# Performance work log

Measured on AMD Instinct MI355X. Metric: run time of the kernel, lower is better.

## Reference

```python
import jax, jax.numpy as jnp
import numpy as np

NEG_INF = -1e12  # matches masked_fill value -1000000000000.0
LEAKY_SLOPE = 0.2


def setup_inputs() -> dict:
    key = jax.random.key(0)
    k1, k2, k3, k4, k5 = jax.random.split(key, 5)
    B, C, H, N, F_IN, F_OUT = 4, 4, 4, 1024, 64, 64
    h = jax.random.normal(k1, (B, C, N, F_IN), dtype=jnp.float32)
    adj = jax.random.randint(k2, (B, N, N), 0, 2).astype(jnp.float32)
    w = jax.random.normal(k3, (C, H, F_IN, F_OUT), dtype=jnp.float32) * 0.1
    a_src = jax.random.normal(k4, (C, H, F_OUT, 1), dtype=jnp.float32) * 0.1
    a_dst = jax.random.normal(k5, (C, H, F_OUT, 1), dtype=jnp.float32) * 0.1
    return {"h": h, "adj": adj, "w": w, "a_src": a_src, "a_dst": a_dst}


def reference(h, adj, w, a_src, a_dst):
    # h: [B,C,N,f_in], w: [C,H,f_in,f_out] -> h_prime: [B,C,H,N,f_out]
    h_prime = jnp.einsum('bcnf,chfo->bchno', h, w)
    t = jnp.tanh(h_prime)
    # additive attention scores: [B,C,H,N]
    attn_src = jnp.einsum('bchno,cho->bchn', t, a_src[..., 0])
    attn_dst = jnp.einsum('bchno,cho->bchn', t, a_dst[..., 0])
    # attn[b,c,h,i,j] = src[i] + dst[j]  -> [B,C,H,N,N]
    attn = attn_src[..., :, None] + attn_dst[..., None, :]
    attn = jnp.where(attn >= 0, attn, LEAKY_SLOPE * attn)  # leaky_relu(0.2)
    N = h.shape[2]
    adj_sl = adj + jnp.eye(N, dtype=adj.dtype)  # add self-loops
    mask = (adj_sl == 0)[:, None, None, :, :]   # [B,1,1,N,N]
    attn = jnp.where(mask, NEG_INF, attn)
    attn = jax.nn.softmax(attn, axis=-1)
    # dropout is identity (attn_dropout=0.0 / eval mode)
    out = jnp.einsum('bchnm,bchmo->bchno', attn, h_prime)
    return out
```

## Files before the change

### kernel.cpp

```cpp
#include <hip/hip_runtime.h>
#include <hip/hip_bf16.h>
#include <math.h>

#define NB 4
#define NC 4
#define NH 4
#define NN 1024
#define NF 64
#define NCOMBO 64
#define LEAK 0.2f

typedef __attribute__((ext_vector_type(8)))  short  short8;
typedef __attribute__((ext_vector_type(16))) float  float16;

static __device__ __forceinline__ unsigned pk_bf16(float a, float b) {
    union { __hip_bfloat162 h; unsigned u; } cv;
    cv.h = __float22bfloat162_rn(make_float2(a, b));
    return cv.u;
}

static __device__ __forceinline__ float fast_tanh(float x) {
    const float e = __expf(2.f * x);
    return 1.f - 2.f * __builtin_amdgcn_rcpf(1.f + e);
}

static __device__ __forceinline__ float mask_by_bit(float p, unsigned bb, int k) {
#if defined(__has_builtin) && __has_builtin(__builtin_amdgcn_sbfe)
    const int m = __builtin_amdgcn_sbfe((int)bb, k, 1);
#else
    const int m = -(int)((bb >> k) & 1u);
#endif
    union { float f; int i; } u;
    u.f = p; u.i &= m;
    return u.f;
}

static __device__ __forceinline__ void split8(const float4 a, const float4 b,
                                              short8* hi, short8* lo) {
    union { short8 v; unsigned u[4]; } H, L;
    const float x[8] = {a.x,a.y,a.z,a.w,b.x,b.y,b.z,b.w};
    float lov[8];
    #pragma unroll
    for (int p = 0; p < 4; ++p) {
        const unsigned pk = pk_bf16(x[2*p], x[2*p+1]);
        H.u[p] = pk;
        union { unsigned u; float f; } f0, f1;
        f0.u = pk << 16; f1.u = pk & 0xffff0000u;
        lov[2*p]   = x[2*p]   - f0.f;
        lov[2*p+1] = x[2*p+1] - f1.f;
    }
    #pragma unroll
    for (int p = 0; p < 4; ++p) L.u[p] = pk_bf16(lov[2*p], lov[2*p+1]);
    *hi = H.v; *lo = L.v;
}

__global__ __launch_bounds__(256) void gA_produce(
    const float* __restrict__ h, const float* __restrict__ adj,
    const float* __restrict__ w, const float* __restrict__ a_src,
    const float* __restrict__ a_dst,
    unsigned short* __restrict__ hpt, float* __restrict__ asrc,
    float* __restrict__ edPt, float* __restrict__ edNt,
    unsigned long long* __restrict__ bits)
{
    __shared__ __align__(16) char smem[17920];
    float* w_s    = (float*)smem;
    unsigned short* whi = (unsigned short*)smem;
    unsigned short* wlo = (unsigned short*)(smem + 8192);
    float* as_lds = (float*)(smem + 16384);
    float* ad_lds = (float*)(smem + 16640);
    float* scS    = (float*)(smem + 16896);
    float* scD    = (float*)(smem + 17408);

    const int idx  = blockIdx.x;
    const int t    = threadIdx.x;
    const int g    = (idx & 7)*8 + ((idx >> 3) & 7);
    const int tile = idx >> 6;
    const int b = g >> 4, c = (g >> 2) & 3, hh = g & 3;
    const int lane = t & 63, l31 = lane & 31, half = lane >> 5;
    const int wv = t >> 6, rg = wv >> 1, oh = wv & 1;

    const float4* wsrc = (const float4*)(w + ((size_t)(c*NH + hh))*NF*NF);
    #pragma unroll
    for (int i = 0; i < 4; ++i)
        ((float4*)w_s)[t + i*256] = wsrc[t + i*256];
    if (t < NF) {
        as_lds[t] = a_src[(c*NH + hh)*NF + t];
        ad_lds[t] = a_dst[(c*NH + hh)*NF + t];
    }
    __syncthreads();

    float wv0[8], wv1[8];
    {
        const int n = t & 31;
        #pragma unroll
        for (int j = 0; j < 8; ++j) {
            const int blk0 = t >> 5, blk1 = (t >> 5) + 8;
            const int k0 = (blk0 >> 2)*16 + (blk0 & 1)*8 + j;
            const int o0 = ((blk0 >> 1) & 1)*32 + n;
            const int k1 = (blk1 >> 2)*16 + (blk1 & 1)*8 + j;
            const int o1 = ((blk1 >> 1) & 1)*32 + n;
            wv0[j] = w_s[k0*64 + o0];
            wv1[j] = w_s[k1*64 + o1];
        }
    }
    short8 ahi[4], alo[4];
    {
        const float* hrow = h +
            (((size_t)(b*NC + c))*NN + tile*64 + rg*32 + l31)*NF;
        #pragma unroll
        for (int s = 0; s < 4; ++s) {
            const float4 v0 = *(const float4*)&hrow[s*16 + half*8];
            const float4 v1 = *(const float4*)&hrow[s*16 + half*8 + 4];
            split8(v0, v1, &ahi[s], &alo[s]);
        }
    }
    __syncthreads();

    {
        union { short8 v; unsigned u[4]; } H; short8 L;
        float4 a0 = make_float4(wv0[0],wv0[1],wv0[2],wv0[3]);
        float4 a1 = make_float4(wv0[4],wv0[5],wv0[6],wv0[7]);
        split8(a0, a1, &H.v, &L);
        *(short8*)&whi[((t >> 5)*32 + (t & 31))*8] = H.v;
        *(short8*)&wlo[((t >> 5)*32 + (t & 31))*8] = L;
        a0 = make_float4(wv1[0],wv1[1],wv1[2],wv1[3]);
        a1 = make_float4(wv1[4],wv1[5],wv1[6],wv1[7]);
        split8(a0, a1, &H.v, &L);
        *(short8*)&whi[(((t >> 5) + 8)*32 + (t & 31))*8] = H.v;
        *(short8*)&wlo[(((t >> 5) + 8)*32 + (t & 31))*8] = L;
    }
    __syncthreads();

    float16 acc;
    #pragma unroll
    for (int i = 0; i < 16; ++i) acc[i] = 0.f;
    #pragma unroll
    for (int s = 0; s < 4; ++s) {
        const short8 bhi = *(const short8*)&whi[(((s*2 + oh)*2 + half)*32 + l31)*8];
        const short8 blo = *(const short8*)&wlo[(((s*2 + oh)*2 + half)*32 + l31)*8];
        acc = __builtin_amdgcn_mfma_f32_32x32x16_bf16(ahi[s], bhi, acc, 0, 0, 0);
        acc = __builtin_amdgcn_mfma_f32_32x32x16_bf16(alo[s], bhi, acc, 0, 0, 0);
        acc = __builtin_amdgcn_mfma_f32_32x32x16_bf16(ahi[s], blo, acc, 0, 0, 0);
    }

    {
        const int col = oh*32 + l31;
        const float av = as_lds[col], dv = ad_lds[col];
        float sS[16], sD[16];
        #pragma unroll
        for (int reg = 0; reg < 16; ++reg) {
            const float tt = fast_tanh(acc[reg]);
            sS[reg] = tt * av;
            sD[reg] = tt * dv;
        }
        #pragma unroll
        for (int off = 1; off <= 16; off <<= 1) {
            #pragma unroll
            for (int reg = 0; reg < 16; ++reg) {
                sS[reg] += __shfl_xor(sS[reg], off);
                sD[reg] += __shfl_xor(sD[reg], off);
            }
        }
        if (l31 == 0) {
            #pragma unroll
            for (int reg = 0; reg < 16; ++reg) {
                const int row = rg*32 + (reg & 3) + 8*(reg >> 2) + 4*half;
                scS[row*2 + oh] = sS[reg];
                scD[row*2 + oh] = sD[reg];
            }
        }
    }

    {
        unsigned short* dst = hpt + ((size_t)(g*16 + tile))*4096;
        #pragma unroll
        for (int q = 0; q < 4; ++q) {
            const int ks = rg*2 + (q >> 1), hf = q & 1;
            const int elem = (((ks*2 + oh)*2 + hf)*32 + l31)*8 + 4*half;
            uint2 pk;
            pk.x = pk_bf16(acc[q*4 + 0], acc[q*4 + 1]);
            pk.y = pk_bf16(acc[q*4 + 2], acc[q*4 + 3]);
            *(uint2*)&dst[elem] = pk;
        }
    }
    __syncthreads();
    if (t < 64) {
        const float s = scS[t*2] + scS[t*2 + 1];
        const float d = scD[t*2] + scD[t*2 + 1];
        asrc[(size_t)g*NN + tile*64 + t] = s;
        edPt[(size_t)g*NN + tile*64 + t] = __expf(d);
        edNt[(size_t)g*NN + tile*64 + t] = __expf(LEAK*d);
    }

    {
        const int base = idx*4096;
        #pragma unroll
        for (int q = 0; q < 16; ++q) {
            const int e  = base + q*256 + t;
            const int j  = e & (NN-1);
            const int i  = (e >> 10) & (NN-1);
            const int bb = e >> 20;
            const bool pred = (adj[e] != 0.f) || (j == i);
            const unsigned long long m = __ballot(pred);
            if ((t & 63) == 0) bits[((size_t)bb*NN + i)*16 + (j >> 6)] = m;
        }
    }
}

__global__ __launch_bounds__(256, 4) void gC_attn(
    const unsigned short* __restrict__ hpt, const float* __restrict__ asrc,
    const float* __restrict__ edPt, const float* __restrict__ edNt,
    const unsigned long long* __restrict__ bits, float* __restrict__ out)
{
    __shared__ __align__(16) char smem[17920];
    float* edP_lds = (float*)smem;
    float* edN_lds = (float*)(smem + 4096);
    unsigned long long* bits_lds = (unsigned long long*)(smem + 8192);
    float* comb  = (float*)smem;
    float* psum2 = (float*)(smem + 17408);

    const int idx = blockIdx.x;
    const int t   = threadIdx.x;
    const int g   = (idx & 7)*8 + ((idx >> 3) & 7);
    const int it  = idx >> 6;
    const int b   = g >> 4;
    const int i0  = it*64;
    const int wv = t >> 6, lane = t & 63;
    const int l31 = lane & 31, half = lane >> 5;
    const int rg = wv >> 1, jh = wv & 1;
    const int myrow = rg*32 + l31;

    #pragma unroll
    for (int q = 0; q < 4; ++q) {
        const int j = q*256 + t;
        edP_lds[j] = edPt[(size_t)g*NN + j];
        edN_lds[j] = edNt[(size_t)g*NN + j];
    }
    {
        const unsigned long long* bsrc = bits + ((size_t)b*NN + i0)*16;
        #pragma unroll
        for (int q = 0; q < 4; ++q) {
            const int e = q*256 + t;
            bits_lds[(e >> 4)*17 + (e & 15)] = bsrc[e];
        }
    }
    const float sv    = asrc[(size_t)g*NN + i0 + myrow];
    const float ratio = __expf((LEAK - 1.f)*sv);
    __syncthreads();

    union { short8 v; unsigned short u[8]; } ONES;
    #pragma unroll
    for (int i = 0; i < 8; ++i) ONES.u[i] = 0x3F80;

    float16 acc0, acc1, acc2;
    #pragma unroll
    for (int i = 0; i < 16; ++i) { acc0[i] = 0.f; acc1[i] = 0.f; acc2[i] = 0.f; }

    const unsigned short* hb = hpt + (size_t)g*16*4096;

    short8 b0, b1;
    {
        const int ks = jh*2;
        b0 = *(const short8*)&hb[(((ks*2 + 0)*2 + half)*32 + l31)*8];
        b1 = *(const short8*)&hb[(((ks*2 + 1)*2 + half)*32 + l31)*8];
    }

    #pragma unroll
    for (int m = 0; m < 32; ++m) {
        const int jt = m >> 1, kk = m & 1;
        const int ks = jh*2 + kk;
        const int jo = ks*16 + half*8;

        short8 nb0, nb1;
        if (m < 31) {
            const int jt1 = (m + 1) >> 1, kk1 = (m + 1) & 1;
            const int ks1 = jh*2 + kk1;
            const size_t base1 = (size_t)jt1*4096;
            nb0 = *(const short8*)&hb[base1 + (((ks1*2 + 0)*2 + half)*32 + l31)*8];
            nb1 = *(const short8*)&hb[base1 + (((ks1*2 + 1)*2 + half)*32 + l31)*8];
        }

        const unsigned long long wb = bits_lds[myrow*17 + jt];
        const unsigned bb = (unsigned)(wb >> jo) & 0xffu;

        const float4 P0 = *(const float4*)&edP_lds[jt*64 + jo];
        const float4 P1 = *(const float4*)&edP_lds[jt*64 + jo + 4];
        const float4 Q0 = *(const float4*)&edN_lds[jt*64 + jo];
        const float4 Q1 = *(const float4*)&edN_lds[jt*64 + jo + 4];
        const float Pp[8] = {P0.x,P0.y,P0.z,P0.w,P1.x,P1.y,P1.z,P1.w};
        const float Nv[8] = {Q0.x,Q0.y,Q0.z,Q0.w,Q1.x,Q1.y,Q1.z,Q1.w};

        float pv[8];
        #pragma unroll
        for (int e2 = 0; e2 < 8; ++e2)
            pv[e2] = mask_by_bit(fmaxf(Pp[e2], ratio*Nv[e2]), bb, e2);

        union { short8 v; unsigned u[4]; } af;
        af.u[0] = pk_bf16(pv[0], pv[1]);
        af.u[1] = pk_bf16(pv[2], pv[3]);
        af.u[2] = pk_bf16(pv[4], pv[5]);
        af.u[3] = pk_bf16(pv[6], pv[7]);

        acc2 = __builtin_amdgcn_mfma_f32_32x32x16_bf16(af.v, ONES.v, acc2, 0, 0, 0);
        acc0 = __builtin_amdgcn_mfma_f32_32x32x16_bf16(af.v, b0,     acc0, 0, 0, 0);
        acc1 = __builtin_amdgcn_mfma_f32_32x32x16_bf16(af.v, b1,     acc1, 0, 0, 0);

        if (m < 31) { b0 = nb0; b1 = nb1; }
    }

    __syncthreads();

    if (l31 == 0) {
        #pragma unroll
        for (int reg = 0; reg < 16; ++reg) {
            const int r = (reg & 3) + 8*(reg >> 2) + 4*half;
            psum2[jh*64 + rg*32 + r] = acc2[reg];
        }
    }
    if (jh == 1) {
        float* cb = comb + (rg*64 + lane)*34;
        #pragma unroll
        for (int i = 0; i < 8; ++i) {
            float2 v0; v0.x = acc0[2*i]; v0.y = acc0[2*i+1];
            float2 v1; v1.x = acc1[2*i]; v1.y = acc1[2*i+1];
            *(float2*)&cb[2*i]      = v0;
            *(float2*)&cb[16 + 2*i] = v1;
        }
    }
    __syncthreads();
    if (jh == 0) {
        const float* cb = comb + (rg*64 + lane)*34;
        #pragma unroll
        for (int i = 0; i < 8; ++i) {
            const float2 v0 = *(const float2*)&cb[2*i];
            const float2 v1 = *(const float2*)&cb[16 + 2*i];
            acc0[2*i] += v0.x; acc0[2*i+1] += v0.y;
            acc1[2*i] += v1.x; acc1[2*i+1] += v1.y;
        }
        #pragma unroll
        for (int reg = 0; reg < 16; ++reg) {
            const int r = (reg & 3) + 8*(reg >> 2) + 4*half;
            const int row = rg*32 + r;
            const float inv = __builtin_amdgcn_rcpf(psum2[row] + psum2[64 + row]);
            const size_t base = ((size_t)g*NN + i0 + row)*NF;
            out[base + l31]      = acc0[reg] * inv;
            out[base + l31 + 32] = acc1[reg] * inv;
        }
    }
}

extern "C" void kernel_launch(void* const* d_in, const int* in_sizes, int n_in,
                              void* d_out, int out_size, void* d_ws, size_t ws_size,
                              hipStream_t stream)
{
    const float* h     = (const float*)d_in[0];
    const float* adj   = (const float*)d_in[1];
    const float* w     = (const float*)d_in[2];
    const float* a_src = (const float*)d_in[3];
    const float* a_dst = (const float*)d_in[4];
    float* out = (float*)d_out;

    char* ws = (char*)d_ws;
    unsigned short* hpt = (unsigned short*)ws;
    float* asrc         = (float*)(ws + 8388608);
    float* edP          = (float*)(ws + 8388608 + 262144);
    float* edN          = (float*)(ws + 8388608 + 524288);
    unsigned long long* bits = (unsigned long long*)(ws + 8388608 + 786432);

    gA_produce<<<dim3(1024), dim3(256), 0, stream>>>(
        h, adj, w, a_src, a_dst, hpt, asrc, edP, edN, bits);
    gC_attn<<<dim3(1024), dim3(256), 0, stream>>>(
        hpt, asrc, edP, edN, bits, out);
}
```

Baseline: 115.5 us.

## Fuse produce and attention kernels into one cooperative launch with grid sync

```diff
diff --git a/kernel.cpp b/kernel.cpp
--- a/kernel.cpp
+++ b/kernel.cpp
@@ -1,5 +1,6 @@
 #include <hip/hip_runtime.h>
 #include <hip/hip_bf16.h>
+#include <hip/hip_cooperative_groups.h>
 #include <math.h>
 
 #define NB 4
@@ -25,11 +26,7 @@
 }
 
 static __device__ __forceinline__ float mask_by_bit(float p, unsigned bb, int k) {
-#if defined(__has_builtin) && __has_builtin(__builtin_amdgcn_sbfe)
-    const int m = __builtin_amdgcn_sbfe((int)bb, k, 1);
-#else
     const int m = -(int)((bb >> k) & 1u);
-#endif
     union { float f; int i; } u;
     u.f = p; u.i &= m;
     return u.f;
@@ -54,7 +51,8 @@
     *hi = H.v; *lo = L.v;
 }
 
-__global__ __launch_bounds__(256) void gA_produce(
+static __device__ __forceinline__ void phaseA(
+    char* smem, const int idx, const int t,
     const float* __restrict__ h, const float* __restrict__ adj,
     const float* __restrict__ w, const float* __restrict__ a_src,
     const float* __restrict__ a_dst,
@@ -62,7 +60,6 @@
     float* __restrict__ edPt, float* __restrict__ edNt,
     unsigned long long* __restrict__ bits)
 {
-    __shared__ __align__(16) char smem[17920];
     float* w_s    = (float*)smem;
     unsigned short* whi = (unsigned short*)smem;
     unsigned short* wlo = (unsigned short*)(smem + 8192);
@@ -71,8 +68,6 @@
     float* scS    = (float*)(smem + 16896);
     float* scD    = (float*)(smem + 17408);
 
-    const int idx  = blockIdx.x;
-    const int t    = threadIdx.x;
     const int g    = (idx & 7)*8 + ((idx >> 3) & 7);
     const int tile = idx >> 6;
     const int b = g >> 4, c = (g >> 2) & 3, hh = g & 3;
@@ -207,20 +202,18 @@
     }
 }
 
-__global__ __launch_bounds__(256, 4) void gC_attn(
+static __device__ __forceinline__ void phaseC(
+    char* smem, const int idx, const int t,
     const unsigned short* __restrict__ hpt, const float* __restrict__ asrc,
     const float* __restrict__ edPt, const float* __restrict__ edNt,
     const unsigned long long* __restrict__ bits, float* __restrict__ out)
 {
-    __shared__ __align__(16) char smem[17920];
     float* edP_lds = (float*)smem;
     float* edN_lds = (float*)(smem + 4096);
     unsigned long long* bits_lds = (unsigned long long*)(smem + 8192);
     float* comb  = (float*)smem;
     float* psum2 = (float*)(smem + 17408);
 
-    const int idx = blockIdx.x;
-    const int t   = threadIdx.x;
     const int g   = (idx & 7)*8 + ((idx >> 3) & 7);
     const int it  = idx >> 6;
     const int b   = g >> 4;
@@ -267,14 +260,14 @@
 
     #pragma unroll
     for (int m = 0; m < 32; ++m) {
-        const int jt = m >> 1, kk = m & 1;
-        const int ks = jh*2 + kk;
+        const int jt = m >> 1;
+        const int ks = jh*2 + (m & 1);
         const int jo = ks*16 + half*8;
 
         short8 nb0, nb1;
         if (m < 31) {
-            const int jt1 = (m + 1) >> 1, kk1 = (m + 1) & 1;
-            const int ks1 = jh*2 + kk1;
+            const int jt1 = (m + 1) >> 1;
+            const int ks1 = jh*2 + ((m + 1) & 1);
             const size_t base1 = (size_t)jt1*4096;
             nb0 = *(const short8*)&hb[base1 + (((ks1*2 + 0)*2 + half)*32 + l31)*8];
             nb1 = *(const short8*)&hb[base1 + (((ks1*2 + 1)*2 + half)*32 + l31)*8];
@@ -349,6 +342,48 @@
     }
 }
 
+__global__ __launch_bounds__(256, 4) void fused_all(
+    const float* __restrict__ h, const float* __restrict__ adj,
+    const float* __restrict__ w, const float* __restrict__ a_src,
+    const float* __restrict__ a_dst,
+    unsigned short* __restrict__ hpt, float* __restrict__ asrc,
+    float* __restrict__ edPt, float* __restrict__ edNt,
+    unsigned long long* __restrict__ bits, float* __restrict__ out)
+{
+    __shared__ __align__(16) char smem[17920];
+    const int idx = blockIdx.x;
+    const int t   = threadIdx.x;
+
+    phaseA(smem, idx, t, h, adj, w, a_src, a_dst, hpt, asrc, edPt, edNt, bits);
+
+    __threadfence();
+    cooperative_groups::this_grid().sync();
+
+    phaseC(smem, idx, t, hpt, asrc, edPt, edNt, bits, out);
+}
+
+__global__ __launch_bounds__(256) void gA_produce(
+    const float* __restrict__ h, const float* __restrict__ adj,
+    const float* __restrict__ w, const float* __restrict__ a_src,
+    const float* __restrict__ a_dst,
+    unsigned short* __restrict__ hpt, float* __restrict__ asrc,
+    float* __restrict__ edPt, float* __restrict__ edNt,
+    unsigned long long* __restrict__ bits)
+{
+    __shared__ __align__(16) char smem[17920];
+    phaseA(smem, blockIdx.x, threadIdx.x, h, adj, w, a_src, a_dst,
+           hpt, asrc, edPt, edNt, bits);
+}
+
+__global__ __launch_bounds__(256, 4) void gC_attn(
+    const unsigned short* __restrict__ hpt, const float* __restrict__ asrc,
+    const float* __restrict__ edPt, const float* __restrict__ edNt,
+    const unsigned long long* __restrict__ bits, float* __restrict__ out)
+{
+    __shared__ __align__(16) char smem[17920];
+    phaseC(smem, blockIdx.x, threadIdx.x, hpt, asrc, edPt, edNt, bits, out);
+}
+
 extern "C" void kernel_launch(void* const* d_in, const int* in_sizes, int n_in,
                               void* d_out, int out_size, void* d_ws, size_t ws_size,
                               hipStream_t stream)
@@ -367,8 +402,34 @@
     float* edN          = (float*)(ws + 8388608 + 524288);
     unsigned long long* bits = (unsigned long long*)(ws + 8388608 + 786432);
 
-    gA_produce<<<dim3(1024), dim3(256), 0, stream>>>(
-        h, adj, w, a_src, a_dst, hpt, asrc, edP, edN, bits);
-    gC_attn<<<dim3(1024), dim3(256), 0, stream>>>(
-        hpt, asrc, edP, edN, bits, out);
-}
+    static int coopOK = -1;
+    if (coopOK < 0) {
+        int attr = 0;
+        if (hipDeviceGetAttribute(&attr, hipDeviceAttributeCooperativeLaunch, 0)
+            != hipSuccess) attr = 0;
+        int maxB = 0;
+        if (hipOccupancyMaxActiveBlocksPerMultiprocessor(
+                &maxB, (const void*)fused_all, 256, 0) != hipSuccess) maxB = 0;
+        coopOK = (attr != 0 && maxB >= 4) ? 1 : 0;
+    }
+
+    bool done = false;
+    if (coopOK == 1) {
+        void* args[] = {(void*)&h, (void*)&adj, (void*)&w, (void*)&a_src,
+                        (void*)&a_dst, (void*)&hpt, (void*)&asrc, (void*)&edP,
+                        (void*)&edN, (void*)&bits, (void*)&out};
+        if (hipLaunchCooperativeKernel((const void*)fused_all, dim3(1024),
+                                       dim3(256), args, 0u, stream)
+            == hipSuccess) {
+            done = true;
+        } else {
+            coopOK = 0;
+        }
+    }
+    if (!done) {
+        gA_produce<<<dim3(1024), dim3(256), 0, stream>>>(
+            h, adj, w, a_src, a_dst, hpt, asrc, edP, edN, bits);
+        gC_attn<<<dim3(1024), dim3(256), 0, stream>>>(
+            hpt, asrc, edP, edN, bits, out);
+    }
+}
```

After: 116.0 us. No clear change (+0.4%).

## Prefetch adjacency early, read weights from global, deepen B-operand prefetch

Applied to the files above, without the earlier changes.

```diff
diff --git a/kernel.cpp b/kernel.cpp
--- a/kernel.cpp
+++ b/kernel.cpp
@@ -25,11 +25,7 @@
 }
 
 static __device__ __forceinline__ float mask_by_bit(float p, unsigned bb, int k) {
-#if defined(__has_builtin) && __has_builtin(__builtin_amdgcn_sbfe)
-    const int m = __builtin_amdgcn_sbfe((int)bb, k, 1);
-#else
     const int m = -(int)((bb >> k) & 1u);
-#endif
     union { float f; int i; } u;
     u.f = p; u.i &= m;
     return u.f;
@@ -63,7 +59,6 @@
     unsigned long long* __restrict__ bits)
 {
     __shared__ __align__(16) char smem[17920];
-    float* w_s    = (float*)smem;
     unsigned short* whi = (unsigned short*)smem;
     unsigned short* wlo = (unsigned short*)(smem + 8192);
     float* as_lds = (float*)(smem + 16384);
@@ -79,16 +74,12 @@
     const int lane = t & 63, l31 = lane & 31, half = lane >> 5;
     const int wv = t >> 6, rg = wv >> 1, oh = wv & 1;
 
-    const float4* wsrc = (const float4*)(w + ((size_t)(c*NH + hh))*NF*NF);
-    #pragma unroll
-    for (int i = 0; i < 4; ++i)
-        ((float4*)w_s)[t + i*256] = wsrc[t + i*256];
-    if (t < NF) {
-        as_lds[t] = a_src[(c*NH + hh)*NF + t];
-        ad_lds[t] = a_dst[(c*NH + hh)*NF + t];
-    }
-    __syncthreads();
-
+    float av16[16];
+    const int abase = idx*4096;
+    #pragma unroll
+    for (int q = 0; q < 16; ++q) av16[q] = adj[abase + q*256 + t];
+
+    const float* wg = w + ((size_t)(c*NH + hh))*NF*NF;
     float wv0[8], wv1[8];
     {
         const int n = t & 31;
@@ -99,10 +90,15 @@
             const int o0 = ((blk0 >> 1) & 1)*32 + n;
             const int k1 = (blk1 >> 2)*16 + (blk1 & 1)*8 + j;
             const int o1 = ((blk1 >> 1) & 1)*32 + n;
-            wv0[j] = w_s[k0*64 + o0];
-            wv1[j] = w_s[k1*64 + o1];
-        }
-    }
+            wv0[j] = wg[k0*64 + o0];
+            wv1[j] = wg[k1*64 + o1];
+        }
+    }
+    if (t < NF) {
+        as_lds[t] = a_src[(c*NH + hh)*NF + t];
+        ad_lds[t] = a_dst[(c*NH + hh)*NF + t];
+    }
+
     short8 ahi[4], alo[4];
     {
         const float* hrow = h +
@@ -114,7 +110,6 @@
             split8(v0, v1, &ahi[s], &alo[s]);
         }
     }
-    __syncthreads();
 
     {
         union { short8 v; unsigned u[4]; } H; short8 L;
@@ -192,18 +187,15 @@
         edNt[(size_t)g*NN + tile*64 + t] = __expf(LEAK*d);
     }
 
-    {
-        const int base = idx*4096;
-        #pragma unroll
-        for (int q = 0; q < 16; ++q) {
-            const int e  = base + q*256 + t;
-            const int j  = e & (NN-1);
-            const int i  = (e >> 10) & (NN-1);
-            const int bb = e >> 20;
-            const bool pred = (adj[e] != 0.f) || (j == i);
-            const unsigned long long m = __ballot(pred);
-            if ((t & 63) == 0) bits[((size_t)bb*NN + i)*16 + (j >> 6)] = m;
-        }
+    #pragma unroll
+    for (int q = 0; q < 16; ++q) {
+        const int e  = abase + q*256 + t;
+        const int j  = e & (NN-1);
+        const int i  = (e >> 10) & (NN-1);
+        const int bb = e >> 20;
+        const bool pred = (av16[q] != 0.f) || (j == i);
+        const unsigned long long m = __ballot(pred);
+        if ((t & 63) == 0) bits[((size_t)bb*NN + i)*16 + (j >> 6)] = m;
     }
 }
 
@@ -258,27 +250,25 @@
 
     const unsigned short* hb = hpt + (size_t)g*16*4096;
 
-    short8 b0, b1;
-    {
-        const int ks = jh*2;
-        b0 = *(const short8*)&hb[(((ks*2 + 0)*2 + half)*32 + l31)*8];
-        b1 = *(const short8*)&hb[(((ks*2 + 1)*2 + half)*32 + l31)*8];
-    }
+    short8 B0[3], B1[3];
+    #define LOADM(slot, mm) do { \
+        const int jt_ = (mm) >> 1; \
+        const int ks_ = jh*2 + ((mm) & 1); \
+        const size_t base_ = (size_t)jt_*4096; \
+        B0[slot] = *(const short8*)&hb[base_ + (((ks_*2 + 0)*2 + half)*32 + l31)*8]; \
+        B1[slot] = *(const short8*)&hb[base_ + (((ks_*2 + 1)*2 + half)*32 + l31)*8]; \
+    } while (0)
+
+    LOADM(0, 0);
+    LOADM(1, 1);
 
     #pragma unroll
     for (int m = 0; m < 32; ++m) {
-        const int jt = m >> 1, kk = m & 1;
-        const int ks = jh*2 + kk;
+        const int jt = m >> 1;
+        const int ks = jh*2 + (m & 1);
         const int jo = ks*16 + half*8;
 
-        short8 nb0, nb1;
-        if (m < 31) {
-            const int jt1 = (m + 1) >> 1, kk1 = (m + 1) & 1;
-            const int ks1 = jh*2 + kk1;
-            const size_t base1 = (size_t)jt1*4096;
-            nb0 = *(const short8*)&hb[base1 + (((ks1*2 + 0)*2 + half)*32 + l31)*8];
-            nb1 = *(const short8*)&hb[base1 + (((ks1*2 + 1)*2 + half)*32 + l31)*8];
-        }
+        if (m + 2 < 32) LOADM((m + 2) % 3, m + 2);
 
         const unsigned long long wb = bits_lds[myrow*17 + jt];
         const unsigned bb = (unsigned)(wb >> jo) & 0xffu;
@@ -302,11 +292,10 @@
         af.u[3] = pk_bf16(pv[6], pv[7]);
 
         acc2 = __builtin_amdgcn_mfma_f32_32x32x16_bf16(af.v, ONES.v, acc2, 0, 0, 0);
-        acc0 = __builtin_amdgcn_mfma_f32_32x32x16_bf16(af.v, b0,     acc0, 0, 0, 0);
-        acc1 = __builtin_amdgcn_mfma_f32_32x32x16_bf16(af.v, b1,     acc1, 0, 0, 0);
-
-        if (m < 31) { b0 = nb0; b1 = nb1; }
-    }
+        acc0 = __builtin_amdgcn_mfma_f32_32x32x16_bf16(af.v, B0[m % 3], acc0, 0, 0, 0);
+        acc1 = __builtin_amdgcn_mfma_f32_32x32x16_bf16(af.v, B1[m % 3], acc1, 0, 0, 0);
+    }
+    #undef LOADM
 
     __syncthreads();
 
```

After: 111.2 us. 3.7% less time.
